# Kernel tuning notes

Measured on AMD Instinct MI355X. Metric: run time of the kernel, lower is better.

The kernel has to match this reference:

```python
import jax, jax.numpy as jnp
import numpy as np

DIM = 768
HEADS = 12
HEAD_DIM = DIM // HEADS
SCALE = HEAD_DIM ** -0.5


def setup_inputs() -> dict:
    key = jax.random.key(0)
    ks = jax.random.split(key, 6)
    B, N, C = 2, 2048, DIM
    x = jax.random.normal(ks[0], (B, N, C), dtype=jnp.float32)
    s = C ** -0.5
    Wq = jax.random.normal(ks[1], (C, C), dtype=jnp.float32) * s
    Wk = jax.random.normal(ks[2], (C, C), dtype=jnp.float32) * s
    Wv = jax.random.normal(ks[3], (C, C), dtype=jnp.float32) * s
    Wp = jax.random.normal(ks[4], (C, C), dtype=jnp.float32) * s
    bp = jax.random.normal(ks[5], (C,), dtype=jnp.float32) * 0.01
    return {"x": x, "Wq": Wq, "Wk": Wk, "Wv": Wv, "Wp": Wp, "bp": bp}


def reference(x, Wq, Wk, Wv, Wp, bp):
    B, N, C = x.shape
    h, d = HEADS, HEAD_DIM
    # projections (no bias), split heads: (B, h, N, d)
    Q = (x @ Wq.T).reshape(B, N, h, d).transpose(0, 2, 1, 3)
    K = (x @ Wk.T).reshape(B, N, h, d).transpose(0, 2, 1, 3)
    V = (x @ Wv.T).reshape(B, N, h, d).transpose(0, 2, 1, 3)
    # averaged key: (B, h, 1, d) -> scores (B, h, N)
    K_avg = K.mean(axis=2)  # (B, h, d)
    z = jnp.einsum('bhnd,bhd->bhn', Q, K_avg) * SCALE
    attn = jax.nn.softmax(z, axis=-1)  # (B, h, N)
    # circulant gather: roll[b,h,i,j] = attn[b,h,(j-i)%N] / N
    idx = (jnp.arange(N)[None, :] - jnp.arange(N)[:, None]) % N  # (N, N)
    roll = attn[:, :, idx] / N  # (B, h, N, N)
    out = jnp.einsum('bhij,bhjd->bhid', roll, V)  # (B, h, N, d)
    out = out.transpose(0, 2, 1, 3).reshape(B, N, C)
    return out @ Wp.T + bp
```

## Files before the change

### kernel.cpp

```cpp
#include <hip/hip_runtime.h>


typedef __bf16 bf16x8 __attribute__((ext_vector_type(8)));
typedef float  f32x4  __attribute__((ext_vector_type(4)));

#define AS_GLOBAL(p) ((const __attribute__((address_space(1))) unsigned int*)(p))
#define AS_LDS(p)    ((__attribute__((address_space(3))) unsigned int*)(p))

__device__ __forceinline__ void async16(const void* g, void* l) {
    __builtin_amdgcn_global_load_lds(AS_GLOBAL(g), AS_LDS(l), 16, 0, 0);
}

struct bf4 { __bf16 a, b, c, d; };

template <int BN, int MODE>
__device__ void gemm_phase(char* smem, const __bf16* __restrict__ A,
                           const __bf16* __restrict__ Bt, void* __restrict__ Cout,
                           const float* __restrict__ bias,
                           int K, int ldA, int ldBt, int ldC, int mBase, int nBase)
{
    constexpr int STRIDE = (128 + BN) * 32 * 2;
    constexpr int WN = BN / 2, NI = WN / 16;
    const int tid = threadIdx.x;
    const int lane = tid & 63, wid = tid >> 6;
    const int lane15 = lane & 15, quad = lane >> 4;
    const int wm = (wid & 1) * 64, wn = (wid >> 1) * WN;

    auto stage = [&](int kb, int buf) {
        __bf16* As = (__bf16*)(smem + buf * STRIDE);
        __bf16* Bs = As + 128 * 32;
#pragma unroll
        for (int c0 = 0; c0 < 512; c0 += 256) {
            int c = c0 + tid, row = c >> 2, slot = c & 3;
            int k8 = slot ^ ((row >> 1) & 3);
            async16(A + (size_t)(mBase + row) * ldA + kb + k8 * 8, As + c * 8);
        }
#pragma unroll
        for (int c0 = 0; c0 < BN * 4; c0 += 256) {
            int c = c0 + tid, row = c >> 2, slot = c & 3;
            int k8 = slot ^ ((row >> 1) & 3);
            async16(Bt + (size_t)(nBase + row) * ldBt + kb + k8 * 8, Bs + c * 8);
        }
    };

    f32x4 acc[4][NI] = {};
    const int nk = K >> 5;

    stage(0, 0);
    for (int ki = 0; ki < nk; ++ki) {
        __syncthreads();
        if (ki + 1 < nk) stage((ki + 1) << 5, (ki + 1) & 1);

        __bf16* As = (__bf16*)(smem + (ki & 1) * STRIDE);
        __bf16* Bs = As + 128 * 32;
        bf16x8 af[4], bv[NI];
#pragma unroll
        for (int mi = 0; mi < 4; ++mi) {
            int row = wm + mi * 16 + lane15;
            af[mi] = *(const bf16x8*)&As[row * 32 + (quad ^ ((row >> 1) & 3)) * 8];
        }
#pragma unroll
        for (int ni = 0; ni < NI; ++ni) {
            int row = wn + ni * 16 + lane15;
            bv[ni] = *(const bf16x8*)&Bs[row * 32 + (quad ^ ((row >> 1) & 3)) * 8];
        }
#pragma unroll
        for (int mi = 0; mi < 4; ++mi)
#pragma unroll
            for (int ni = 0; ni < NI; ++ni)
                acc[mi][ni] = __builtin_amdgcn_mfma_f32_16x16x32_bf16(
                    af[mi], bv[ni], acc[mi][ni], 0, 0, 0);
    }

#pragma unroll
    for (int mi = 0; mi < 4; ++mi)
#pragma unroll
        for (int ni = 0; ni < NI; ++ni)
#pragma unroll
            for (int r = 0; r < 4; ++r) {
                int row = mBase + wm + mi * 16 + quad * 4 + r;
                int col = nBase + wn + ni * 16 + lane15;
                float v = acc[mi][ni][r];
                if (MODE == 0) {
                    ((__bf16*)Cout)[(size_t)row * ldC + col] = (__bf16)v;
                } else if (MODE == 1) {
                    ((float*)Cout)[(size_t)row * ldC + col] = v + bias[col];
                } else {
                    int b = row >> 11;
                    if ((unsigned)(col - b * 12) < 12u)
                        ((float*)Cout)[(size_t)col * 2048 + (row & 2047)] = v;
                }
            }
}

__global__ __launch_bounds__(256)
void k_prep(const float* __restrict__ x, const float* __restrict__ Wv,
            const float* __restrict__ Wp,
            __bf16* __restrict__ xb, __bf16* __restrict__ Wvb,
            __bf16* __restrict__ Wpb, float* __restrict__ x_avg)
{
    const int bid = blockIdx.x, tid = threadIdx.x;
    __shared__ float sums[768];
    for (int c = tid; c < 768; c += 256) sums[c] = 0.f;
    __syncthreads();

    const float4* xs = (const float4*)x + (size_t)bid * 1536;
    bf4* xd = (bf4*)xb + (size_t)bid * 1536;
#pragma unroll
    for (int r = 0; r < 6; ++r) {
        int j = tid + r * 256;
        float4 v = xs[j];
        xd[j] = bf4{(__bf16)v.x, (__bf16)v.y, (__bf16)v.z, (__bf16)v.w};
        int col = (j % 192) * 4;
        atomicAdd(&sums[col + 0], v.x);
        atomicAdd(&sums[col + 1], v.y);
        atomicAdd(&sums[col + 2], v.z);
        atomicAdd(&sums[col + 3], v.w);
    }
    const float4* wv4 = (const float4*)Wv;  bf4* wvb4 = (bf4*)Wvb;
    const float4* wp4 = (const float4*)Wp;  bf4* wpb4 = (bf4*)Wpb;
    for (int t = tid; t < 288; t += 256) {
        int g = bid * 288 + t;
        float4 v = wv4[g];
        wvb4[g] = bf4{(__bf16)v.x, (__bf16)v.y, (__bf16)v.z, (__bf16)v.w};
        float4 w2 = wp4[g];
        wpb4[g] = bf4{(__bf16)w2.x, (__bf16)w2.y, (__bf16)w2.z, (__bf16)w2.w};
    }
    __syncthreads();
    const int b = bid >> 8;
    for (int c = tid; c < 768; c += 256)
        atomicAdd(&x_avg[b * 768 + c], sums[c]);
}

__global__ __launch_bounds__(256)
void k_ub(const float* __restrict__ x_avg, const float* __restrict__ Wk,
          const float* __restrict__ Wq, __bf16* __restrict__ Ub)
{
    const int bid = blockIdx.x, tid = threadIdx.x;
    const int lane = tid & 63, wid = tid >> 6;
    __shared__ float sx[768];
    __shared__ float sk[64];
    int b = bid / 12, h = bid % 12;
    for (int c = tid; c < 768; c += 256) sx[c] = x_avg[b * 768 + c];
    __syncthreads();
    for (int round = 0; round < 16; ++round) {
        int o = round * 4 + wid;
        const float* wk = Wk + (size_t)(h * 64 + o) * 768;
        float s = 0.f;
#pragma unroll
        for (int cc0 = 0; cc0 < 768; cc0 += 64) s += sx[cc0 + lane] * wk[cc0 + lane];
#pragma unroll
        for (int off = 32; off; off >>= 1) s += __shfl_down(s, off);
        if (lane == 0) sk[o] = s * (0.125f / 2048.f);
    }
    __syncthreads();
    for (int c = tid; c < 768; c += 256) {
        float s = 0.f;
#pragma unroll 16
        for (int d2 = 0; d2 < 64; ++d2)
            s += sk[d2] * Wq[(size_t)(h * 64 + d2) * 768 + c];
        Ub[(size_t)bid * 768 + c] = (__bf16)s;
    }
}

__global__ __launch_bounds__(256, 2)
void k_gemms(const __bf16* __restrict__ xb, const __bf16* __restrict__ Wvb,
             const __bf16* __restrict__ Ub, __bf16* __restrict__ VT,
             float* __restrict__ z_t)
{
    __shared__ __attribute__((aligned(16))) char smem[32768];
    const int bid = blockIdx.x;
    if (bid < 192) {
        gemm_phase<128, 0>(smem, Wvb, xb, VT, nullptr, 768, 768, 768, 4096,
                           (bid / 32) * 128, (bid % 32) * 128);
    } else {
        gemm_phase<64, 2>(smem, xb, Ub, z_t, nullptr, 768, 768, 768, 0,
                          (bid - 192) * 128, 0);
    }
}

__global__ __launch_bounds__(256, 2)
void k_conv(const float* __restrict__ z_t, const __bf16* __restrict__ VT,
            __bf16* __restrict__ outp)
{
    __shared__ __attribute__((aligned(16))) char smem[53376];
    __bf16 (*rep)[2056] = (__bf16(*)[2056])smem;
    float* red = (float*)(smem + 32896);
    __bf16* attn_s = (__bf16*)(smem + 49280);

    const int bid = blockIdx.x, tid = threadIdx.x;
    const int lane = tid & 63, wid = tid >> 6;
    const int lane15 = lane & 15, quad = lane >> 4;
    const int bh = bid >> 3, b = bh / 12, h = bh % 12;
    const int m0 = (bid & 7) * 256 + wid * 64;

    {
        const float* z = z_t + (size_t)bh * 2048;
        float v[8];
        float m = -1e30f;
#pragma unroll
        for (int j = 0; j < 8; ++j) { v[j] = z[tid + j * 256]; m = fmaxf(m, v[j]); }
#pragma unroll
        for (int off = 32; off; off >>= 1) m = fmaxf(m, __shfl_xor(m, off));
        if (lane == 0) red[wid] = m;
        __syncthreads();
        m = fmaxf(fmaxf(red[0], red[1]), fmaxf(red[2], red[3]));
        __syncthreads();
        float s = 0.f;
#pragma unroll
        for (int j = 0; j < 8; ++j) { v[j] = __expf(v[j] - m); s += v[j]; }
#pragma unroll
        for (int off = 32; off; off >>= 1) s += __shfl_xor(s, off);
        if (lane == 0) red[wid] = s;
        __syncthreads();
        s = red[0] + red[1] + red[2] + red[3];
        float inv = 1.f / (s * 2048.f);
#pragma unroll
        for (int j = 0; j < 8; ++j)
            attn_s[tid + j * 256] = (__bf16)(v[j] * inv);
    }
    __syncthreads();
    for (int idx = tid; idx < 8 * 2048; idx += 256) {
        int a = idx >> 11, u = idx & 2047;
        rep[a][u] = attn_s[(u + a) & 2047];
    }

    const __bf16* vsrc = VT + (size_t)h * 64 * 4096 + b * 2048;

    auto stage = [&](int kb, int buf) {
        __bf16* vt = (__bf16*)(smem + 32896 + buf * 8192);
#pragma unroll
        for (int c0 = 0; c0 < 512; c0 += 256) {
            int c = c0 + tid, dd = c >> 3, slot = c & 7;
            int k8 = slot ^ (dd & 7);
            async16(vsrc + (size_t)dd * 4096 + kb * 64 + k8 * 8, vt + c * 8);
        }
    };

    f32x4 acc[4][4] = {};
    stage(0, 0);
    for (int kb = 0; kb < 32; ++kb) {
        __syncthreads();
        if (kb + 1 < 32) stage(kb + 1, (kb + 1) & 1);
        __bf16* vt = (__bf16*)(smem + 32896 + (kb & 1) * 8192);

#pragma unroll
        for (int ks = 0; ks < 2; ++ks) {
            int kloc = ks * 32 + quad * 8;
            int kglob = kb * 64 + kloc;
            bf16x8 af[4], bv[4];
#pragma unroll
            for (int mi = 0; mi < 4; ++mi) {
                int m = m0 + mi * 16 + lane15;
                int p = (kglob - m) & 2047;
                int al = p & 7;
                af[mi] = *(const bf16x8*)&rep[al][p - al];
            }
#pragma unroll
            for (int ni = 0; ni < 4; ++ni) {
                int dd = ni * 16 + lane15;
                int slot = (kloc >> 3) ^ (dd & 7);
                bv[ni] = *(const bf16x8*)&vt[dd * 64 + slot * 8];
            }
#pragma unroll
            for (int mi = 0; mi < 4; ++mi)
#pragma unroll
                for (int ni = 0; ni < 4; ++ni)
                    acc[mi][ni] = __builtin_amdgcn_mfma_f32_16x16x32_bf16(
                        af[mi], bv[ni], acc[mi][ni], 0, 0, 0);
        }
    }

#pragma unroll
    for (int mi = 0; mi < 4; ++mi)
#pragma unroll
        for (int ni = 0; ni < 4; ++ni)
#pragma unroll
            for (int r = 0; r < 4; ++r) {
                int i = m0 + mi * 16 + quad * 4 + r;
                int dd = ni * 16 + lane15;
                outp[(size_t)(b * 2048 + i) * 768 + h * 64 + dd] =
                    (__bf16)acc[mi][ni][r];
            }
}

__global__ __launch_bounds__(256, 2)
void k_out(const __bf16* __restrict__ out_pre, const __bf16* __restrict__ Wpb,
           const float* __restrict__ bp, float* __restrict__ out)
{
    __shared__ __attribute__((aligned(16))) char smem[32768];
    const int bid = blockIdx.x;
    gemm_phase<128, 1>(smem, out_pre, Wpb, out, bp, 768, 768, 768, 768,
                       (bid / 6) * 128, (bid % 6) * 128);
}

extern "C" void kernel_launch(void* const* d_in, const int* in_sizes, int n_in,
                              void* d_out, int out_size, void* d_ws, size_t ws_size,
                              hipStream_t stream)
{
    (void)in_sizes; (void)n_in; (void)out_size; (void)ws_size;
    const float* x  = (const float*)d_in[0];
    const float* Wq = (const float*)d_in[1];
    const float* Wk = (const float*)d_in[2];
    const float* Wv = (const float*)d_in[3];
    const float* Wp = (const float*)d_in[4];
    const float* bp = (const float*)d_in[5];

    char* w = (char*)d_ws;
    auto alloc = [&](size_t bytes) {
        char* p = w; w += (bytes + 255) & ~(size_t)255; return p;
    };
    float*  x_avg   = (float*) alloc((size_t)2 * 768 * 4);
    __bf16* xb      = (__bf16*)alloc((size_t)4096 * 768 * 2);
    __bf16* Wvb     = (__bf16*)alloc((size_t)768 * 768 * 2);
    __bf16* Wpb     = (__bf16*)alloc((size_t)768 * 768 * 2);
    __bf16* Ub      = (__bf16*)alloc((size_t)64 * 768 * 2);
    float*  z_t     = (float*) alloc((size_t)24 * 2048 * 4);
    __bf16* VT      = (__bf16*)alloc((size_t)768 * 4096 * 2);
    __bf16* out_pre = (__bf16*)alloc((size_t)4096 * 768 * 2);

    hipMemsetAsync(x_avg, 0, 2 * 768 * sizeof(float), stream);
    k_prep <<<512, 256, 0, stream>>>(x, Wv, Wp, xb, Wvb, Wpb, x_avg);
    k_ub   <<<24,  256, 0, stream>>>(x_avg, Wk, Wq, Ub);
    k_gemms<<<224, 256, 0, stream>>>(xb, Wvb, Ub, VT, z_t);
    k_conv <<<192, 256, 0, stream>>>(z_t, VT, out_pre);
    k_out  <<<192, 256, 0, stream>>>(out_pre, Wpb, bp, (float*)d_out);
}
```

Baseline: 169.6 us.

## Double GEMM K-tile to 64 and split conv work across more blocks

```diff
diff --git a/kernel.cpp b/kernel.cpp
--- a/kernel.cpp
+++ b/kernel.cpp
@@ -13,67 +13,72 @@
 
 struct bf4 { __bf16 a, b, c, d; };
 
-template <int BN, int MODE>
+template <int BM, int BN, int MODE>
 __device__ void gemm_phase(char* smem, const __bf16* __restrict__ A,
                            const __bf16* __restrict__ Bt, void* __restrict__ Cout,
                            const float* __restrict__ bias,
                            int K, int ldA, int ldBt, int ldC, int mBase, int nBase)
 {
-    constexpr int STRIDE = (128 + BN) * 32 * 2;
-    constexpr int WN = BN / 2, NI = WN / 16;
+    constexpr int BK = 64;
+    constexpr int STRIDE = (BM + BN) * BK * 2;
+    constexpr int WM = BM / 2, WN = BN / 2;
+    constexpr int MI = WM / 16, NI = WN / 16;
     const int tid = threadIdx.x;
     const int lane = tid & 63, wid = tid >> 6;
     const int lane15 = lane & 15, quad = lane >> 4;
-    const int wm = (wid & 1) * 64, wn = (wid >> 1) * WN;
+    const int wm = (wid & 1) * WM, wn = (wid >> 1) * WN;
 
     auto stage = [&](int kb, int buf) {
         __bf16* As = (__bf16*)(smem + buf * STRIDE);
-        __bf16* Bs = As + 128 * 32;
-#pragma unroll
-        for (int c0 = 0; c0 < 512; c0 += 256) {
-            int c = c0 + tid, row = c >> 2, slot = c & 3;
-            int k8 = slot ^ ((row >> 1) & 3);
+        __bf16* Bs = As + BM * BK;
+#pragma unroll
+        for (int c0 = 0; c0 < BM * 8; c0 += 256) {
+            int c = c0 + tid, row = c >> 3, slot = c & 7;
+            int k8 = slot ^ (row & 7);
             async16(A + (size_t)(mBase + row) * ldA + kb + k8 * 8, As + c * 8);
         }
 #pragma unroll
-        for (int c0 = 0; c0 < BN * 4; c0 += 256) {
-            int c = c0 + tid, row = c >> 2, slot = c & 3;
-            int k8 = slot ^ ((row >> 1) & 3);
+        for (int c0 = 0; c0 < BN * 8; c0 += 256) {
+            int c = c0 + tid, row = c >> 3, slot = c & 7;
+            int k8 = slot ^ (row & 7);
             async16(Bt + (size_t)(nBase + row) * ldBt + kb + k8 * 8, Bs + c * 8);
         }
     };
 
-    f32x4 acc[4][NI] = {};
-    const int nk = K >> 5;
+    f32x4 acc[MI][NI] = {};
+    const int nk = K >> 6;
 
     stage(0, 0);
     for (int ki = 0; ki < nk; ++ki) {
         __syncthreads();
-        if (ki + 1 < nk) stage((ki + 1) << 5, (ki + 1) & 1);
+        if (ki + 1 < nk) stage((ki + 1) << 6, (ki + 1) & 1);
 
         __bf16* As = (__bf16*)(smem + (ki & 1) * STRIDE);
-        __bf16* Bs = As + 128 * 32;
-        bf16x8 af[4], bv[NI];
-#pragma unroll
-        for (int mi = 0; mi < 4; ++mi) {
-            int row = wm + mi * 16 + lane15;
-            af[mi] = *(const bf16x8*)&As[row * 32 + (quad ^ ((row >> 1) & 3)) * 8];
-        }
-#pragma unroll
-        for (int ni = 0; ni < NI; ++ni) {
-            int row = wn + ni * 16 + lane15;
-            bv[ni] = *(const bf16x8*)&Bs[row * 32 + (quad ^ ((row >> 1) & 3)) * 8];
-        }
-#pragma unroll
-        for (int mi = 0; mi < 4; ++mi)
-#pragma unroll
-            for (int ni = 0; ni < NI; ++ni)
-                acc[mi][ni] = __builtin_amdgcn_mfma_f32_16x16x32_bf16(
-                    af[mi], bv[ni], acc[mi][ni], 0, 0, 0);
-    }
-
-#pragma unroll
-    for (int mi = 0; mi < 4; ++mi)
+        __bf16* Bs = As + BM * BK;
+#pragma unroll
+        for (int ks = 0; ks < 2; ++ks) {
+            bf16x8 af[MI], bv[NI];
+#pragma unroll
+            for (int mi = 0; mi < MI; ++mi) {
+                int row = wm + mi * 16 + lane15;
+                af[mi] = *(const bf16x8*)&As[row * 64 + ((ks * 4 + quad) ^ (row & 7)) * 8];
+            }
+#pragma unroll
+            for (int ni = 0; ni < NI; ++ni) {
+                int row = wn + ni * 16 + lane15;
+                bv[ni] = *(const bf16x8*)&Bs[row * 64 + ((ks * 4 + quad) ^ (row & 7)) * 8];
+            }
+#pragma unroll
+            for (int mi = 0; mi < MI; ++mi)
+#pragma unroll
+                for (int ni = 0; ni < NI; ++ni)
+                    acc[mi][ni] = __builtin_amdgcn_mfma_f32_16x16x32_bf16(
+                        af[mi], bv[ni], acc[mi][ni], 0, 0, 0);
+        }
+    }
+
+#pragma unroll
+    for (int mi = 0; mi < MI; ++mi)
 #pragma unroll
         for (int ni = 0; ni < NI; ++ni)
 #pragma unroll
@@ -168,14 +173,14 @@
              const __bf16* __restrict__ Ub, __bf16* __restrict__ VT,
              float* __restrict__ z_t)
 {
-    __shared__ __attribute__((aligned(16))) char smem[32768];
+    __shared__ __attribute__((aligned(16))) char smem[65536];
     const int bid = blockIdx.x;
     if (bid < 192) {
-        gemm_phase<128, 0>(smem, Wvb, xb, VT, nullptr, 768, 768, 768, 4096,
-                           (bid / 32) * 128, (bid % 32) * 128);
+        gemm_phase<128, 128, 0>(smem, Wvb, xb, VT, nullptr, 768, 768, 768, 4096,
+                                (bid / 32) * 128, (bid % 32) * 128);
     } else {
-        gemm_phase<64, 2>(smem, xb, Ub, z_t, nullptr, 768, 768, 768, 0,
-                          (bid - 192) * 128, 0);
+        gemm_phase<128, 64, 2>(smem, xb, Ub, z_t, nullptr, 768, 768, 768, 0,
+                               (bid - 192) * 128, 0);
     }
 }
 
@@ -183,16 +188,17 @@
 void k_conv(const float* __restrict__ z_t, const __bf16* __restrict__ VT,
             __bf16* __restrict__ outp)
 {
-    __shared__ __attribute__((aligned(16))) char smem[53376];
+    __shared__ __attribute__((aligned(16))) char smem[69760];
     __bf16 (*rep)[2056] = (__bf16(*)[2056])smem;
     float* red = (float*)(smem + 32896);
-    __bf16* attn_s = (__bf16*)(smem + 49280);
+    __bf16* attn_s = (__bf16*)(smem + 65664);
 
     const int bid = blockIdx.x, tid = threadIdx.x;
     const int lane = tid & 63, wid = tid >> 6;
     const int lane15 = lane & 15, quad = lane >> 4;
-    const int bh = bid >> 3, b = bh / 12, h = bh % 12;
-    const int m0 = (bid & 7) * 256 + wid * 64;
+    const int bh = bid >> 4, b = bh / 12, h = bh % 12;
+    const int m0 = (bid & 15) * 128 + (wid & 1) * 64;
+    const int wn = (wid >> 1) * 32;
 
     {
         const float* z = z_t + (size_t)bh * 2048;
@@ -228,27 +234,27 @@
     const __bf16* vsrc = VT + (size_t)h * 64 * 4096 + b * 2048;
 
     auto stage = [&](int kb, int buf) {
-        __bf16* vt = (__bf16*)(smem + 32896 + buf * 8192);
-#pragma unroll
-        for (int c0 = 0; c0 < 512; c0 += 256) {
-            int c = c0 + tid, dd = c >> 3, slot = c & 7;
-            int k8 = slot ^ (dd & 7);
-            async16(vsrc + (size_t)dd * 4096 + kb * 64 + k8 * 8, vt + c * 8);
+        __bf16* vt = (__bf16*)(smem + 32896 + buf * 16384);
+#pragma unroll
+        for (int c0 = 0; c0 < 1024; c0 += 256) {
+            int c = c0 + tid, dd = c >> 4, slot = c & 15;
+            int k8 = slot ^ (dd & 15);
+            async16(vsrc + (size_t)dd * 4096 + kb * 128 + k8 * 8, vt + c * 8);
         }
     };
 
-    f32x4 acc[4][4] = {};
+    f32x4 acc[4][2] = {};
     stage(0, 0);
-    for (int kb = 0; kb < 32; ++kb) {
-        __syncthreads();
-        if (kb + 1 < 32) stage(kb + 1, (kb + 1) & 1);
-        __bf16* vt = (__bf16*)(smem + 32896 + (kb & 1) * 8192);
-
-#pragma unroll
-        for (int ks = 0; ks < 2; ++ks) {
+    for (int kb = 0; kb < 16; ++kb) {
+        __syncthreads();
+        if (kb + 1 < 16) stage(kb + 1, (kb + 1) & 1);
+        __bf16* vt = (__bf16*)(smem + 32896 + (kb & 1) * 16384);
+
+#pragma unroll
+        for (int ks = 0; ks < 4; ++ks) {
             int kloc = ks * 32 + quad * 8;
-            int kglob = kb * 64 + kloc;
-            bf16x8 af[4], bv[4];
+            int kglob = kb * 128 + kloc;
+            bf16x8 af[4], bv[2];
 #pragma unroll
             for (int mi = 0; mi < 4; ++mi) {
                 int m = m0 + mi * 16 + lane15;
@@ -257,15 +263,15 @@
                 af[mi] = *(const bf16x8*)&rep[al][p - al];
             }
 #pragma unroll
-            for (int ni = 0; ni < 4; ++ni) {
-                int dd = ni * 16 + lane15;
-                int slot = (kloc >> 3) ^ (dd & 7);
-                bv[ni] = *(const bf16x8*)&vt[dd * 64 + slot * 8];
+            for (int ni = 0; ni < 2; ++ni) {
+                int dd = wn + ni * 16 + lane15;
+                int slot = (ks * 4 + quad) ^ (dd & 15);
+                bv[ni] = *(const bf16x8*)&vt[dd * 128 + slot * 8];
             }
 #pragma unroll
             for (int mi = 0; mi < 4; ++mi)
 #pragma unroll
-                for (int ni = 0; ni < 4; ++ni)
+                for (int ni = 0; ni < 2; ++ni)
                     acc[mi][ni] = __builtin_amdgcn_mfma_f32_16x16x32_bf16(
                         af[mi], bv[ni], acc[mi][ni], 0, 0, 0);
         }
@@ -274,11 +280,11 @@
 #pragma unroll
     for (int mi = 0; mi < 4; ++mi)
 #pragma unroll
-        for (int ni = 0; ni < 4; ++ni)
+        for (int ni = 0; ni < 2; ++ni)
 #pragma unroll
             for (int r = 0; r < 4; ++r) {
                 int i = m0 + mi * 16 + quad * 4 + r;
-                int dd = ni * 16 + lane15;
+                int dd = wn + ni * 16 + lane15;
                 outp[(size_t)(b * 2048 + i) * 768 + h * 64 + dd] =
                     (__bf16)acc[mi][ni][r];
             }
@@ -288,10 +294,10 @@
 void k_out(const __bf16* __restrict__ out_pre, const __bf16* __restrict__ Wpb,
            const float* __restrict__ bp, float* __restrict__ out)
 {
-    __shared__ __attribute__((aligned(16))) char smem[32768];
+    __shared__ __attribute__((aligned(16))) char smem[65536];
     const int bid = blockIdx.x;
-    gemm_phase<128, 1>(smem, out_pre, Wpb, out, bp, 768, 768, 768, 768,
-                       (bid / 6) * 128, (bid % 6) * 128);
+    gemm_phase<128, 128, 1>(smem, out_pre, Wpb, out, bp, 768, 768, 768, 768,
+                            (bid / 6) * 128, (bid % 6) * 128);
 }
 
 extern "C" void kernel_launch(void* const* d_in, const int* in_sizes, int n_in,
@@ -323,6 +329,6 @@
     k_prep <<<512, 256, 0, stream>>>(x, Wv, Wp, xb, Wvb, Wpb, x_avg);
     k_ub   <<<24,  256, 0, stream>>>(x_avg, Wk, Wq, Ub);
     k_gemms<<<224, 256, 0, stream>>>(xb, Wvb, Ub, VT, z_t);
-    k_conv <<<192, 256, 0, stream>>>(z_t, VT, out_pre);
+    k_conv <<<384, 256, 0, stream>>>(z_t, VT, out_pre);
     k_out  <<<192, 256, 0, stream>>>(out_pre, Wpb, bp, (float*)d_out);
 }
```

Result: faster. 159.7 us (-5.8%).
